# Optimization experiments

Measured on AMD Instinct MI355X. Metric: run time of the kernel, lower is better.

The kernel has to match this reference:

```python
import jax, jax.numpy as jnp
import numpy as np

N = 16384
L = 4096  # n_locations

def setup_inputs() -> dict:
    key = jax.random.key(0)
    k1, k2, k3, k4 = jax.random.split(key, 4)
    w = jax.random.randint(k1, (N,), 0, L)
    z = jax.random.normal(k2, (N, L), dtype=jnp.float32)
    W = jax.random.normal(k3, (L, L), dtype=jnp.float32) * (1.0 / np.sqrt(L))
    b = jax.random.normal(k4, (L,), dtype=jnp.float32) * 0.01
    return {"w": w, "z": z, "W": W, "b": b}

def reference(w, z, W, b):
    # zw[i] = z[i, w[i]]
    zw = jnp.take_along_axis(z, w[:, None], axis=1)[:, 0]  # [N]
    # Original: inp = scatter(zw at column w); out = inp @ W.T + b
    # Mathematically: out[i, j] = zw[i] * W[j, w[i]] + b[j]
    out = zw[:, None] * W.T[w] + b  # [N, L]
    return out
```

## Files before the change

kernel.cpp:

```cpp
#include <hip/hip_runtime.h>

#define N_ROWS 16384
#define L_DIM  4096
#define CG     16
#define JT     1024
#define PASS   1024
#define NPASS  (N_ROWS / PASS)
#define PITCH  (JT + 4)

__global__ __launch_bounds__(256, 2) void pnet_fused(
    const int* __restrict__ w,
    const float* __restrict__ z,
    const float* __restrict__ W,
    const float* __restrict__ b,
    float* __restrict__ out)
{
    __shared__ float tile[CG * PITCH];
    __shared__ int   list[PASS];
    __shared__ float zlist[PASS];
    __shared__ int   cnt[NPASS];

    const int tid = threadIdx.x;
    const int l0  = blockIdx.x * CG;
    const int j0  = blockIdx.y * JT;

    if (tid < NPASS) cnt[tid] = 0;

    {
        const int q     = tid & 3;
        const int rbase = tid >> 2;
        #pragma unroll
        for (int it = 0; it < JT / 64; ++it) {
            const int r = rbase + it * 64;
            const float4 v = *(const float4*)&W[(size_t)(j0 + r) * L_DIM + l0 + 4 * q];
            tile[(4 * q + 0) * PITCH + r] = v.x;
            tile[(4 * q + 1) * PITCH + r] = v.y;
            tile[(4 * q + 2) * PITCH + r] = v.z;
            tile[(4 * q + 3) * PITCH + r] = v.w;
        }
    }

    const int wid  = tid >> 6;
    const int lane = tid & 63;
    float4 bb[4];
    #pragma unroll
    for (int k = 0; k < 4; ++k)
        bb[k] = *(const float4*)&b[j0 + (k * 64 + lane) * 4];

    __syncthreads();

    for (int p = 0; p < NPASS; ++p) {
        {
            const int i0  = p * PASS + tid * 4;
            const int4 wv = *(const int4*)&w[i0];
            const int vals[4] = {wv.x, wv.y, wv.z, wv.w};
            #pragma unroll
            for (int e = 0; e < 4; ++e) {
                const unsigned c = (unsigned)(vals[e] - l0);
                if (c < CG) {
                    const int i   = i0 + e;
                    const int pos = atomicAdd(&cnt[p], 1);
                    list[pos]  = i | ((int)c << 16);
                    zlist[pos] = z[(size_t)i * L_DIM + vals[e]];
                }
            }
        }
        __syncthreads();

        const int n = cnt[p];
        for (int e = wid; e < n; e += 4) {
            const int   packed = list[e];
            const int   i      = packed & 0xFFFF;
            const int   c      = packed >> 16;
            const float zw     = zlist[e];
            const float* trow  = &tile[c * PITCH];
            float*       orow  = &out[(size_t)i * L_DIM + j0];
            #pragma unroll
            for (int k = 0; k < 4; ++k) {
                const int jj = (k * 64 + lane) * 4;
                const float4 wv4 = *(const float4*)&trow[jj];
                float4 o;
                o.x = fmaf(zw, wv4.x, bb[k].x);
                o.y = fmaf(zw, wv4.y, bb[k].y);
                o.z = fmaf(zw, wv4.z, bb[k].z);
                o.w = fmaf(zw, wv4.w, bb[k].w);
                *(float4*)&orow[jj] = o;
            }
        }
        __syncthreads();
    }
}

extern "C" void kernel_launch(void* const* d_in, const int* in_sizes, int n_in,
                              void* d_out, int out_size, void* d_ws, size_t ws_size,
                              hipStream_t stream) {
    const int*   w = (const int*)d_in[0];
    const float* z = (const float*)d_in[1];
    const float* W = (const float*)d_in[2];
    const float* b = (const float*)d_in[3];
    float* out = (float*)d_out;

    dim3 grid(L_DIM / CG, L_DIM / JT);
    pnet_fused<<<grid, 256, 0, stream>>>(w, z, W, b, out);
}
```

Before: 74.85 us.

## Prebucket rows by column group in a separate kernel before the main pass

Replaces the per-block scan of all 16384 w entries (16 passes with shared atomics and syncs in each of 1024 blocks) with a global bucketing kernel that fills per-bucket lists of (row, column, zw) in workspace. The main kernel then reads only its own bucket's entries and writes output rows with no per-pass barriers. This removes redundant reads of w across blocks and the sync overhead, at the cost of two extra kernel launches, global atomics, and dependence on workspace capacity (entries beyond cap are silently dropped).

```diff
diff --git a/kernel.cpp b/kernel.cpp
--- a/kernel.cpp
+++ b/kernel.cpp
@@ -4,27 +4,37 @@
 #define L_DIM  4096
 #define CG     16
 #define JT     1024
-#define PASS   1024
-#define NPASS  (N_ROWS / PASS)
+#define NBKT   (L_DIM / CG)
 #define PITCH  (JT + 4)
 
-__global__ __launch_bounds__(256, 2) void pnet_fused(
-    const int* __restrict__ w,
-    const float* __restrict__ z,
-    const float* __restrict__ W,
-    const float* __restrict__ b,
-    float* __restrict__ out)
-{
+__global__ void zero_cnt(int* __restrict__ cnt) { cnt[threadIdx.x] = 0; }
+
+__global__ __launch_bounds__(256) void bucket_k(const int* __restrict__ w,
+                                                const float* __restrict__ z,
+                                                int* __restrict__ cnt,
+                                                int2* __restrict__ entries,
+                                                int cap) {
+    const int i   = blockIdx.x * 256 + threadIdx.x;
+    const int wi  = w[i];
+    const float zw = z[(size_t)i * L_DIM + wi];
+    const int bkt = wi >> 4;
+    const int c   = wi & (CG - 1);
+    const int pos = atomicAdd(&cnt[bkt], 1);
+    if (pos < cap)
+        entries[(size_t)bkt * cap + pos] = make_int2(i | (c << 16), __float_as_int(zw));
+}
+
+__global__ __launch_bounds__(256, 2) void pnet_main(const float* __restrict__ W,
+                                                    const float* __restrict__ b,
+                                                    const int* __restrict__ cnt,
+                                                    const int2* __restrict__ entries,
+                                                    float* __restrict__ out,
+                                                    int cap) {
     __shared__ float tile[CG * PITCH];
-    __shared__ int   list[PASS];
-    __shared__ float zlist[PASS];
-    __shared__ int   cnt[NPASS];
-
+    const int bkt = blockIdx.x;
+    const int l0  = bkt * CG;
+    const int j0  = blockIdx.y * JT;
     const int tid = threadIdx.x;
-    const int l0  = blockIdx.x * CG;
-    const int j0  = blockIdx.y * JT;
-
-    if (tid < NPASS) cnt[tid] = 0;
 
     {
         const int q     = tid & 3;
@@ -47,47 +57,30 @@
     for (int k = 0; k < 4; ++k)
         bb[k] = *(const float4*)&b[j0 + (k * 64 + lane) * 4];
 
+    int n = cnt[bkt];
+    if (n > cap) n = cap;
+
     __syncthreads();
 
-    for (int p = 0; p < NPASS; ++p) {
-        {
-            const int i0  = p * PASS + tid * 4;
-            const int4 wv = *(const int4*)&w[i0];
-            const int vals[4] = {wv.x, wv.y, wv.z, wv.w};
-            #pragma unroll
-            for (int e = 0; e < 4; ++e) {
-                const unsigned c = (unsigned)(vals[e] - l0);
-                if (c < CG) {
-                    const int i   = i0 + e;
-                    const int pos = atomicAdd(&cnt[p], 1);
-                    list[pos]  = i | ((int)c << 16);
-                    zlist[pos] = z[(size_t)i * L_DIM + vals[e]];
-                }
-            }
+    const int2* __restrict__ bl = &entries[(size_t)bkt * cap];
+    for (int e = wid; e < n; e += 4) {
+        const int2  ent = bl[e];
+        const int   i   = ent.x & 0xFFFF;
+        const int   c   = ent.x >> 16;
+        const float zw  = __int_as_float(ent.y);
+        const float* __restrict__ trow = &tile[c * PITCH];
+        float*       __restrict__ orow = &out[(size_t)i * L_DIM + j0];
+        #pragma unroll
+        for (int k = 0; k < 4; ++k) {
+            const int jj = (k * 64 + lane) * 4;
+            const float4 wv4 = *(const float4*)&trow[jj];
+            float4 o;
+            o.x = fmaf(zw, wv4.x, bb[k].x);
+            o.y = fmaf(zw, wv4.y, bb[k].y);
+            o.z = fmaf(zw, wv4.z, bb[k].z);
+            o.w = fmaf(zw, wv4.w, bb[k].w);
+            *(float4*)&orow[jj] = o;
         }
-        __syncthreads();
-
-        const int n = cnt[p];
-        for (int e = wid; e < n; e += 4) {
-            const int   packed = list[e];
-            const int   i      = packed & 0xFFFF;
-            const int   c      = packed >> 16;
-            const float zw     = zlist[e];
-            const float* trow  = &tile[c * PITCH];
-            float*       orow  = &out[(size_t)i * L_DIM + j0];
-            #pragma unroll
-            for (int k = 0; k < 4; ++k) {
-                const int jj = (k * 64 + lane) * 4;
-                const float4 wv4 = *(const float4*)&trow[jj];
-                float4 o;
-                o.x = fmaf(zw, wv4.x, bb[k].x);
-                o.y = fmaf(zw, wv4.y, bb[k].y);
-                o.z = fmaf(zw, wv4.z, bb[k].z);
-                o.w = fmaf(zw, wv4.w, bb[k].w);
-                *(float4*)&orow[jj] = o;
-            }
-        }
-        __syncthreads();
     }
 }
 
@@ -100,6 +93,14 @@
     const float* b = (const float*)d_in[3];
     float* out = (float*)d_out;
 
-    dim3 grid(L_DIM / CG, L_DIM / JT);
-    pnet_fused<<<grid, 256, 0, stream>>>(w, z, W, b, out);
+    int*  cnt     = (int*)d_ws;
+    int2* entries = (int2*)((char*)d_ws + 1024);
+
+    size_t cap_sz = (ws_size - 1024) / ((size_t)NBKT * sizeof(int2));
+    int cap = (cap_sz > N_ROWS) ? N_ROWS : (int)cap_sz;
+
+    zero_cnt<<<1, NBKT, 0, stream>>>(cnt);
+    bucket_k<<<N_ROWS / 256, 256, 0, stream>>>(w, z, cnt, entries, cap);
+    dim3 grid(NBKT, L_DIM / JT);
+    pnet_main<<<grid, 256, 0, stream>>>(W, b, cnt, entries, out, cap);
 }
```

Measured after the change: 86.89 us. 1.16x slower.

## Build full row bucket in one pass before tile load, drop per-pass syncs

Applied to the files above, without the earlier changes.

Scans all of w once to build a single shared-memory list of matching rows (capacity 1792) instead of 16 passes with barriers between them. The scan and the gathered z loads are issued before the W tile transpose, so their latency overlaps with the tile load. Index and z value are packed into one int2 entry. A fallback multi-pass path runs if a bucket overflows. Shared memory use grows, which may affect occupancy.

```diff
diff --git a/kernel.cpp b/kernel.cpp
--- a/kernel.cpp
+++ b/kernel.cpp
@@ -4,9 +4,9 @@
 #define L_DIM  4096
 #define CG     16
 #define JT     1024
-#define PASS   1024
-#define NPASS  (N_ROWS / PASS)
+#define NBKT   (L_DIM / CG)
 #define PITCH  (JT + 4)
+#define CAP    1792
 
 __global__ __launch_bounds__(256, 2) void pnet_fused(
     const int* __restrict__ w,
@@ -16,15 +16,40 @@
     float* __restrict__ out)
 {
     __shared__ float tile[CG * PITCH];
-    __shared__ int   list[PASS];
-    __shared__ float zlist[PASS];
-    __shared__ int   cnt[NPASS];
+    __shared__ int2  list[CAP];
+    __shared__ int   cnt;
 
-    const int tid = threadIdx.x;
-    const int l0  = blockIdx.x * CG;
-    const int j0  = blockIdx.y * JT;
+    const int tid  = threadIdx.x;
+    const int l0   = blockIdx.x * CG;
+    const int j0   = blockIdx.y * JT;
+    const int wid  = tid >> 6;
+    const int lane = tid & 63;
 
-    if (tid < NPASS) cnt[tid] = 0;
+    if (tid == 0) cnt = 0;
+
+    float4 bb[4];
+    #pragma unroll
+    for (int k = 0; k < 4; ++k)
+        bb[k] = *(const float4*)&b[j0 + (k * 64 + lane) * 4];
+
+    __syncthreads();
+
+    #pragma unroll
+    for (int s = 0; s < N_ROWS / 1024; ++s) {
+        const int i0  = s * 1024 + tid * 4;
+        const int4 wv = *(const int4*)&w[i0];
+        const int vals[4] = {wv.x, wv.y, wv.z, wv.w};
+        #pragma unroll
+        for (int e = 0; e < 4; ++e) {
+            const unsigned c = (unsigned)(vals[e] - l0);
+            if (c < CG) {
+                const int pos = atomicAdd(&cnt, 1);
+                if (pos < CAP)
+                    list[pos] = make_int2((i0 + e) | ((int)c << 16),
+                                          __float_as_int(z[(size_t)(i0 + e) * L_DIM + vals[e]]));
+            }
+        }
+    }
 
     {
         const int q     = tid & 3;
@@ -40,54 +65,69 @@
         }
     }
 
-    const int wid  = tid >> 6;
-    const int lane = tid & 63;
-    float4 bb[4];
-    #pragma unroll
-    for (int k = 0; k < 4; ++k)
-        bb[k] = *(const float4*)&b[j0 + (k * 64 + lane) * 4];
+    __syncthreads();
+    const int n     = cnt;
+    const int nmain = n < CAP ? n : CAP;
 
-    __syncthreads();
+    for (int e = wid; e < nmain; e += 4) {
+        const int2  ent = list[e];
+        const int   i   = ent.x & 0xFFFF;
+        const int   c   = ent.x >> 16;
+        const float zw  = __int_as_float(ent.y);
+        const float* __restrict__ trow = &tile[c * PITCH];
+        float*       __restrict__ orow = &out[(size_t)i * L_DIM + j0];
+        #pragma unroll
+        for (int k = 0; k < 4; ++k) {
+            const int jj = (k * 64 + lane) * 4;
+            const float4 wv4 = *(const float4*)&trow[jj];
+            float4 o;
+            o.x = fmaf(zw, wv4.x, bb[k].x);
+            o.y = fmaf(zw, wv4.y, bb[k].y);
+            o.z = fmaf(zw, wv4.z, bb[k].z);
+            o.w = fmaf(zw, wv4.w, bb[k].w);
+            *(float4*)&orow[jj] = o;
+        }
+    }
 
-    for (int p = 0; p < NPASS; ++p) {
-        {
-            const int i0  = p * PASS + tid * 4;
+    if (n > CAP) {
+        for (int p = 0; p < N_ROWS / 1024; ++p) {
+            __syncthreads();
+            if (tid == 0) cnt = 0;
+            __syncthreads();
+            const int i0  = p * 1024 + tid * 4;
             const int4 wv = *(const int4*)&w[i0];
             const int vals[4] = {wv.x, wv.y, wv.z, wv.w};
             #pragma unroll
             for (int e = 0; e < 4; ++e) {
                 const unsigned c = (unsigned)(vals[e] - l0);
                 if (c < CG) {
-                    const int i   = i0 + e;
-                    const int pos = atomicAdd(&cnt[p], 1);
-                    list[pos]  = i | ((int)c << 16);
-                    zlist[pos] = z[(size_t)i * L_DIM + vals[e]];
+                    const int pos = atomicAdd(&cnt, 1);
+                    list[pos] = make_int2((i0 + e) | ((int)c << 16),
+                                          __float_as_int(z[(size_t)(i0 + e) * L_DIM + vals[e]]));
+                }
+            }
+            __syncthreads();
+            const int np = cnt;
+            for (int e = wid; e < np; e += 4) {
+                const int2  ent = list[e];
+                const int   i   = ent.x & 0xFFFF;
+                const int   c   = ent.x >> 16;
+                const float zw  = __int_as_float(ent.y);
+                const float* __restrict__ trow = &tile[c * PITCH];
+                float*       __restrict__ orow = &out[(size_t)i * L_DIM + j0];
+                #pragma unroll
+                for (int k = 0; k < 4; ++k) {
+                    const int jj = (k * 64 + lane) * 4;
+                    const float4 wv4 = *(const float4*)&trow[jj];
+                    float4 o;
+                    o.x = fmaf(zw, wv4.x, bb[k].x);
+                    o.y = fmaf(zw, wv4.y, bb[k].y);
+                    o.z = fmaf(zw, wv4.z, bb[k].z);
+                    o.w = fmaf(zw, wv4.w, bb[k].w);
+                    *(float4*)&orow[jj] = o;
                 }
             }
         }
-        __syncthreads();
-
-        const int n = cnt[p];
-        for (int e = wid; e < n; e += 4) {
-            const int   packed = list[e];
-            const int   i      = packed & 0xFFFF;
-            const int   c      = packed >> 16;
-            const float zw     = zlist[e];
-            const float* trow  = &tile[c * PITCH];
-            float*       orow  = &out[(size_t)i * L_DIM + j0];
-            #pragma unroll
-            for (int k = 0; k < 4; ++k) {
-                const int jj = (k * 64 + lane) * 4;
-                const float4 wv4 = *(const float4*)&trow[jj];
-                float4 o;
-                o.x = fmaf(zw, wv4.x, bb[k].x);
-                o.y = fmaf(zw, wv4.y, bb[k].y);
-                o.z = fmaf(zw, wv4.z, bb[k].z);
-                o.w = fmaf(zw, wv4.w, bb[k].w);
-                *(float4*)&orow[jj] = o;
-            }
-        }
-        __syncthreads();
     }
 }
 
@@ -100,6 +140,6 @@
     const float* b = (const float*)d_in[3];
     float* out = (float*)d_out;
 
-    dim3 grid(L_DIM / CG, L_DIM / JT);
+    dim3 grid(NBKT, L_DIM / JT);
     pnet_fused<<<grid, 256, 0, stream>>>(w, z, W, b, out);
 }
```

Measured after the change: 79.22 us. 5.8% more time.
